# Kernel optimization log

Measured on AMD Instinct MI355X. Metric: run time of the kernel, lower is better.

## Reference

```python
import jax, jax.numpy as jnp
import numpy as np

N_NODES = 50000
N_EDGES = 800000
D = 64
E_DIM = 16
N_GRAPHS = 5000
BN_EPS = 1e-5


def _xavier(key, shape):
    fan_in, fan_out = shape[0], shape[1]
    limit = np.sqrt(6.0 / (fan_in + fan_out))
    return jax.random.uniform(key, shape, jnp.float32, -limit, limit)


def setup_inputs() -> dict:
    key = jax.random.key(0)
    ks = jax.random.split(key, 16)
    x = jax.random.normal(ks[0], (N_NODES, D), jnp.float32)
    edge_index = jax.random.randint(ks[1], (2, N_EDGES), 0, N_NODES, jnp.int64)
    edge_attr = jax.random.normal(ks[2], (N_EDGES, E_DIM), jnp.float32)
    batch = jnp.sort(jax.random.randint(ks[3], (N_NODES,), 0, N_GRAPHS, jnp.int64))
    zdim = 2 * D + E_DIM  # 144
    params = {
        'fw0': _xavier(ks[4], (zdim, D)), 'fb0': jnp.zeros((D,), jnp.float32),
        'sw0': _xavier(ks[5], (zdim, D)), 'sb0': jnp.zeros((D,), jnp.float32),
        'bng0': jnp.ones((D,), jnp.float32), 'bnb0': jnp.zeros((D,), jnp.float32),
        'fw1': _xavier(ks[6], (zdim, D)), 'fb1': jnp.zeros((D,), jnp.float32),
        'sw1': _xavier(ks[7], (zdim, D)), 'sb1': jnp.zeros((D,), jnp.float32),
        'bng1': jnp.ones((D,), jnp.float32), 'bnb1': jnp.zeros((D,), jnp.float32),
        'pw1': _xavier(ks[8], (D, D)), 'pb1': jnp.zeros((D,), jnp.float32),
        'pw2': _xavier(ks[9], (D, D)), 'pb2': jnp.zeros((D,), jnp.float32),
    }
    return dict(x=x, edge_index=edge_index, edge_attr=edge_attr, batch=batch, **params)


def _cgconv(x, src, dst, e, Wf, bf, Ws, bs):
    # PyG CGConv: x_i' = x_i + sum_j sigmoid(Wf z) * softplus(Ws z), z=[x_i, x_j, e]
    # edge_index[0]=source j, edge_index[1]=target i; aggregate at target.
    z = jnp.concatenate([x[dst], x[src], e], axis=-1)  # [E, 2D+Ed]
    m = jax.nn.sigmoid(z @ Wf + bf) * jax.nn.softplus(z @ Ws + bs)  # [E, D]
    agg = jax.ops.segment_sum(m, dst, num_segments=x.shape[0])
    return x + agg


def _batchnorm(x, gamma, beta):
    mu = jnp.mean(x, axis=0)
    var = jnp.mean(jnp.square(x - mu), axis=0)  # biased, training-mode BN
    return (x - mu) * jax.lax.rsqrt(var + BN_EPS) * gamma + beta


def reference(x, edge_index, edge_attr, batch,
              fw0, fb0, sw0, sb0, bng0, bnb0,
              fw1, fb1, sw1, sb1, bng1, bnb1,
              pw1, pb1, pw2, pb2):
    src, dst = edge_index[0], edge_index[1]
    h = _batchnorm(_cgconv(x, src, dst, edge_attr, fw0, fb0, sw0, sb0), bng0, bnb0)
    h = _batchnorm(_cgconv(h, src, dst, edge_attr, fw1, fb1, sw1, sb1), bng1, bnb1)
    # global mean pool over graphs
    sums = jax.ops.segment_sum(h, batch, num_segments=N_GRAPHS)
    cnt = jax.ops.segment_sum(jnp.ones((h.shape[0],), h.dtype), batch, num_segments=N_GRAPHS)
    pooled = sums / jnp.maximum(cnt, 1.0)[:, None]  # [G, D]
    # proj head: Linear -> LeakyReLU(0.01) -> Linear
    y = jax.nn.leaky_relu(pooled @ pw1 + pb1, negative_slope=0.01)
    return y @ pw2 + pb2
```

## Files before the change

### kernel.cpp

```cpp
#include <hip/hip_runtime.h>

#define NN 50000
#define NE 800000
#define DD 64
#define ED 16
#define NG 5000
#define SS 32

__global__ __launch_bounds__(256) void prep_weights(
    const float* __restrict__ fw0, const float* __restrict__ sw0,
    const float* __restrict__ fw1, const float* __restrict__ sw1,
    float2* __restrict__ Wd0, float2* __restrict__ Wsc0, float2* __restrict__ We0,
    float2* __restrict__ Wd1, float2* __restrict__ Wsc1, float2* __restrict__ We1) {
  int i = blockIdx.x * 256 + threadIdx.x;
  if (i >= 2 * 144 * 64) return;
  int layer = i >= 144 * 64;
  int j = i - layer * 144 * 64;
  int k = j >> 6, d = j & 63;
  const float* fw = layer ? fw1 : fw0;
  const float* sw = layer ? sw1 : sw0;
  float2 v = make_float2(fw[j], sw[j]);
  float2* Wd = layer ? Wd1 : Wd0;
  float2* Wsc = layer ? Wsc1 : Wsc0;
  float2* We = layer ? We1 : We0;
  if (k < 64)       Wd[k * DD + d] = v;
  else if (k < 128) Wsc[(k - 64) * DD + d] = v;
  else              We[(k - 128) * DD + d] = v;
}

__global__ __launch_bounds__(256) void k_hist(const int* __restrict__ ei,
                                              int* __restrict__ deg) {
  int e = blockIdx.x * 256 + threadIdx.x;
  if (e < NE) atomicAdd(&deg[ei[NE + e]], 1);
}

__global__ __launch_bounds__(256) void k_scan1(const int* __restrict__ deg,
                                               int* __restrict__ rowptr,
                                               int* __restrict__ partials) {
  __shared__ int sm[256];
  int t = threadIdx.x, i = blockIdx.x * 256 + t;
  int v = (i < NN) ? deg[i] : 0;
  sm[t] = v; __syncthreads();
  for (int off = 1; off < 256; off <<= 1) {
    int x = (t >= off) ? sm[t - off] : 0;
    __syncthreads();
    sm[t] += x;
    __syncthreads();
  }
  if (i < NN) rowptr[i] = sm[t] - v;
  if (t == 255) partials[blockIdx.x] = sm[255];
}

__global__ __launch_bounds__(256) void k_scan2(int* __restrict__ partials,
                                               int* __restrict__ poff, int nparts) {
  __shared__ int sm[256];
  int t = threadIdx.x;
  int v = (t < nparts) ? partials[t] : 0;
  sm[t] = v; __syncthreads();
  for (int off = 1; off < 256; off <<= 1) {
    int x = (t >= off) ? sm[t - off] : 0;
    __syncthreads();
    sm[t] += x;
    __syncthreads();
  }
  poff[t] = sm[t] - v;
}

__global__ __launch_bounds__(256) void k_scan3(int* __restrict__ rowptr,
                                               int* __restrict__ cursor,
                                               const int* __restrict__ poff) {
  int i = blockIdx.x * 256 + threadIdx.x;
  if (i < NN) {
    int v = rowptr[i] + poff[blockIdx.x];
    rowptr[i] = v;
    cursor[i] = v;
  } else if (i == NN) {
    rowptr[NN] = NE;
  }
}

__global__ __launch_bounds__(256) void k_scatter(const int* __restrict__ ei,
                                                 const float4* __restrict__ ea4,
                                                 int* __restrict__ cursor,
                                                 int* __restrict__ ssrc,
                                                 int* __restrict__ sdst,
                                                 float4* __restrict__ sea4) {
  int e = blockIdx.x * 256 + threadIdx.x;
  if (e >= NE) return;
  int dst = ei[NE + e];
  int pos = atomicAdd(&cursor[dst], 1);
  ssrc[pos] = ei[e];
  sdst[pos] = dst;
  const float4* q = ea4 + (size_t)e * 4;
  float4 a0 = q[0], a1 = q[1], a2 = q[2], a3 = q[3];
  float4* o = sea4 + (size_t)pos * 4;
  o[0] = a0; o[1] = a1; o[2] = a2; o[3] = a3;
}

template <int BN>
__global__ __launch_bounds__(256) void node_transform(
    const float* __restrict__ hin, const float* __restrict__ stats,
    const float* __restrict__ gamma, const float* __restrict__ beta,
    const float2* __restrict__ Wd, const float2* __restrict__ Wsc,
    const float* __restrict__ bf, const float* __restrict__ sbv,
    float2* __restrict__ Dst, float2* __restrict__ Src,
    float* __restrict__ hcopy) {
  __shared__ float hrow[32][DD];
  int tid = threadIdx.x, w = tid >> 6, d = tid & 63;
  int nbase = blockIdx.x * 32;
  const float invN = 1.f / (float)NN;
#pragma unroll
  for (int j = 0; j < 2; ++j) {
    int i4 = tid + j * 256;
    int node = nbase + (i4 >> 4);
    if (node < NN) {
      int c = (i4 & 15) * 4;
      float4 v = *(const float4*)(hin + (size_t)node * DD + c);
      if (BN) {
        float mu0 = stats[c + 0] * invN, va0 = stats[64 + c + 0] * invN - mu0 * mu0;
        float mu1 = stats[c + 1] * invN, va1 = stats[64 + c + 1] * invN - mu1 * mu1;
        float mu2 = stats[c + 2] * invN, va2 = stats[64 + c + 2] * invN - mu2 * mu2;
        float mu3 = stats[c + 3] * invN, va3 = stats[64 + c + 3] * invN - mu3 * mu3;
        float sc0 = rsqrtf(va0 + 1e-5f) * gamma[c + 0];
        float sc1 = rsqrtf(va1 + 1e-5f) * gamma[c + 1];
        float sc2 = rsqrtf(va2 + 1e-5f) * gamma[c + 2];
        float sc3 = rsqrtf(va3 + 1e-5f) * gamma[c + 3];
        v.x = fmaf(v.x, sc0, beta[c + 0] - mu0 * sc0);
        v.y = fmaf(v.y, sc1, beta[c + 1] - mu1 * sc1);
        v.z = fmaf(v.z, sc2, beta[c + 2] - mu2 * sc2);
        v.w = fmaf(v.w, sc3, beta[c + 3] - mu3 * sc3);
      }
      *(float4*)(&hrow[i4 >> 4][c]) = v;
      *(float4*)(hcopy + (size_t)node * DD + c) = v;
    }
  }
  __syncthreads();

  float bfd = bf[d], sbd = sbv[d];
  float2 ad[8], as_[8];
#pragma unroll
  for (int i = 0; i < 8; ++i) { ad[i] = make_float2(bfd, sbd); as_[i] = make_float2(0.f, 0.f); }

  for (int kk = 0; kk < 16; ++kk) {
    int k0 = kk * 4;
    float2 wd0 = Wd[(k0 + 0) * DD + d], wd1 = Wd[(k0 + 1) * DD + d];
    float2 wd2 = Wd[(k0 + 2) * DD + d], wd3 = Wd[(k0 + 3) * DD + d];
    float2 ws0 = Wsc[(k0 + 0) * DD + d], ws1 = Wsc[(k0 + 1) * DD + d];
    float2 ws2 = Wsc[(k0 + 2) * DD + d], ws3 = Wsc[(k0 + 3) * DD + d];
#pragma unroll
    for (int i = 0; i < 8; ++i) {
      float4 hv = *(const float4*)(&hrow[w * 8 + i][k0]);
      ad[i].x = fmaf(hv.x, wd0.x, ad[i].x); ad[i].y = fmaf(hv.x, wd0.y, ad[i].y);
      as_[i].x = fmaf(hv.x, ws0.x, as_[i].x); as_[i].y = fmaf(hv.x, ws0.y, as_[i].y);
      ad[i].x = fmaf(hv.y, wd1.x, ad[i].x); ad[i].y = fmaf(hv.y, wd1.y, ad[i].y);
      as_[i].x = fmaf(hv.y, ws1.x, as_[i].x); as_[i].y = fmaf(hv.y, ws1.y, as_[i].y);
      ad[i].x = fmaf(hv.z, wd2.x, ad[i].x); ad[i].y = fmaf(hv.z, wd2.y, ad[i].y);
      as_[i].x = fmaf(hv.z, ws2.x, as_[i].x); as_[i].y = fmaf(hv.z, ws2.y, as_[i].y);
      ad[i].x = fmaf(hv.w, wd3.x, ad[i].x); ad[i].y = fmaf(hv.w, wd3.y, ad[i].y);
      as_[i].x = fmaf(hv.w, ws3.x, as_[i].x); as_[i].y = fmaf(hv.w, ws3.y, as_[i].y);
    }
  }
#pragma unroll
  for (int i = 0; i < 8; ++i) {
    int n = nbase + w * 8 + i;
    if (n < NN) {
      Dst[(size_t)n * DD + d] = ad[i];
      Src[(size_t)n * DD + d] = as_[i];
    }
  }
}

__global__ __launch_bounds__(256, 6) void conv_strip(
    const int* __restrict__ ssrc, const int* __restrict__ sdst,
    const float4* __restrict__ sea4, const float2* __restrict__ We,
    const float2* __restrict__ Dst, const float2* __restrict__ Src,
    float* __restrict__ out) {
  __shared__ float4 sEA[4][SS * 4];
  __shared__ int sid[4][2 * SS];
  int tid = threadIdx.x, w = tid >> 6, d = tid & 63;
  int strip = blockIdx.x * 4 + w;
  int base = strip * SS;

  sEA[w][d]      = sea4[(size_t)base * 4 + d];
  sEA[w][64 + d] = sea4[(size_t)base * 4 + 64 + d];
  sid[w][d] = (d < SS) ? ssrc[base + d] : sdst[base + (d - SS)];
  __syncthreads();

  float2 we[16];
#pragma unroll
  for (int k = 0; k < 16; ++k) we[k] = We[k * DD + d];

  const char* SrcB = (const char*)Src;
  const char* DstB = (const char*)Dst;
  unsigned doff = (unsigned)d * 8u;

#define LOADSRC(n) (*(const float2*)(SrcB + (((unsigned)(n)) << 9) + doff))
#define LOADDST(n) (*(const float2*)(DstB + (((unsigned)(n)) << 9) + doff))

  float2 bufA[4], bufB[4];
#pragma unroll
  for (int j = 0; j < 4; ++j) bufA[j] = LOADSRC(sid[w][j]);

  int curdst = sid[w][SS];
  float2 a = LOADDST(curdst);
  float acc = 0.f;

#pragma unroll
  for (int g = 0; g < SS / 4; ++g) {
    float2* cur = (g & 1) ? bufB : bufA;
    float2* nxt = (g & 1) ? bufA : bufB;
    if (g < SS / 4 - 1) {
#pragma unroll
      for (int j = 0; j < 4; ++j) nxt[j] = LOADSRC(sid[w][g * 4 + 4 + j]);
    }
#pragma unroll
    for (int j = 0; j < 4; ++j) {
      int i = g * 4 + j;
      int dstn = sid[w][SS + i];
      if (dstn != curdst) {
        atomicAdd(&out[(unsigned)curdst * 64u + (unsigned)d], acc);
        acc = 0.f;
        curdst = dstn;
        a = LOADDST(curdst);
      }
      float2 b = cur[j];
      float cf = a.x + b.x, cs = a.y + b.y;
#pragma unroll
      for (int k = 0; k < 4; ++k) {
        float4 z = sEA[w][i * 4 + k];
        cf = fmaf(z.x, we[4 * k + 0].x, cf); cs = fmaf(z.x, we[4 * k + 0].y, cs);
        cf = fmaf(z.y, we[4 * k + 1].x, cf); cs = fmaf(z.y, we[4 * k + 1].y, cs);
        cf = fmaf(z.z, we[4 * k + 2].x, cf); cs = fmaf(z.z, we[4 * k + 2].y, cs);
        cf = fmaf(z.w, we[4 * k + 3].x, cf); cs = fmaf(z.w, we[4 * k + 3].y, cs);
      }
      float sig = __builtin_amdgcn_rcpf(1.f + __expf(-cf));
      float sp  = fmaxf(cs, 0.f) + __logf(1.f + __expf(-fabsf(cs)));
      acc = fmaf(sig, sp, acc);
    }
  }
  atomicAdd(&out[(unsigned)curdst * 64u + (unsigned)d], acc);
#undef LOADSRC
#undef LOADDST
}

__global__ __launch_bounds__(256) void bn_stats(const float* __restrict__ h,
                                                float* __restrict__ stats) {
  int tid = threadIdx.x;
  int c = (tid & 15) * 4;
  int r0 = blockIdx.x * 16 + (tid >> 4);
  float4 s = make_float4(0, 0, 0, 0), ss = make_float4(0, 0, 0, 0);
  for (int r = r0; r < NN; r += gridDim.x * 16) {
    float4 v = *(const float4*)(h + (size_t)r * DD + c);
    s.x += v.x; s.y += v.y; s.z += v.z; s.w += v.w;
    ss.x += v.x * v.x; ss.y += v.y * v.y; ss.z += v.z * v.z; ss.w += v.w * v.w;
  }
  __shared__ float4 sm[256], sm2[256];
  sm[tid] = s; sm2[tid] = ss;
  __syncthreads();
  for (int str = 128; str >= 16; str >>= 1) {
    if (tid < str) {
      sm[tid].x += sm[tid + str].x; sm[tid].y += sm[tid + str].y;
      sm[tid].z += sm[tid + str].z; sm[tid].w += sm[tid + str].w;
      sm2[tid].x += sm2[tid + str].x; sm2[tid].y += sm2[tid + str].y;
      sm2[tid].z += sm2[tid + str].z; sm2[tid].w += sm2[tid + str].w;
    }
    __syncthreads();
  }
  if (tid < 16) {
    int cc = tid * 4;
    atomicAdd(&stats[cc + 0], sm[tid].x); atomicAdd(&stats[cc + 1], sm[tid].y);
    atomicAdd(&stats[cc + 2], sm[tid].z); atomicAdd(&stats[cc + 3], sm[tid].w);
    atomicAdd(&stats[64 + cc + 0], sm2[tid].x); atomicAdd(&stats[64 + cc + 1], sm2[tid].y);
    atomicAdd(&stats[64 + cc + 2], sm2[tid].z); atomicAdd(&stats[64 + cc + 3], sm2[tid].w);
  }
}

__global__ __launch_bounds__(256) void pool_bn(
    const float* __restrict__ h, const int* __restrict__ batch,
    const float* __restrict__ stats,
    const float* __restrict__ gamma, const float* __restrict__ beta,
    float* __restrict__ psum, float* __restrict__ pcnt) {
  int tid = threadIdx.x, g = tid >> 6, d = tid & 63;
  const float invN = 1.f / (float)NN;
  float mu = stats[d] * invN;
  float var = stats[64 + d] * invN - mu * mu;
  float sc = rsqrtf(var + 1e-5f) * gamma[d];
  float sh = beta[d] - mu * sc;
  int n0 = (blockIdx.x * 4 + g) * 32;
  if (n0 >= NN) return;
  int nend = n0 + 32; if (nend > NN) nend = NN;
  int bprev = batch[n0];
  float acc = 0.f; int run = 0;
  for (int n = n0; n < nend; ++n) {
    int b = batch[n];
    if (b != bprev) {
      atomicAdd(&psum[(size_t)bprev * DD + d], acc);
      if (d == 0) atomicAdd(&pcnt[bprev], (float)run);
      acc = 0.f; run = 0; bprev = b;
    }
    acc += fmaf(h[(size_t)n * DD + d], sc, sh);
    ++run;
  }
  atomicAdd(&psum[(size_t)bprev * DD + d], acc);
  if (d == 0) atomicAdd(&pcnt[bprev], (float)run);
}

__global__ __launch_bounds__(256) void head_kernel(
    const float* __restrict__ psum, const float* __restrict__ pcnt,
    const float* __restrict__ pw1, const float* __restrict__ pb1,
    const float* __restrict__ pw2, const float* __restrict__ pb2,
    float* __restrict__ out) {
  __shared__ float row[4][DD], y1[4][DD];
  int tid = threadIdx.x, g = tid >> 6, d = tid & 63;
  int q = blockIdx.x * 4 + g;
  float c = fmaxf(pcnt[q], 1.0f);
  row[g][d] = psum[(size_t)q * DD + d] * __builtin_amdgcn_rcpf(c);
  __syncthreads();
  float acc = pb1[d];
#pragma unroll
  for (int k = 0; k < DD; ++k) acc = fmaf(row[g][k], pw1[k * DD + d], acc);
  acc = acc > 0.f ? acc : 0.01f * acc;
  y1[g][d] = acc;
  __syncthreads();
  float o = pb2[d];
#pragma unroll
  for (int k = 0; k < DD; ++k) o = fmaf(y1[g][k], pw2[k * DD + d], o);
  out[(size_t)q * DD + d] = o;
}

extern "C" void kernel_launch(void* const* d_in, const int* in_sizes, int n_in,
                              void* d_out, int out_size, void* d_ws, size_t ws_size,
                              hipStream_t stream) {
  const float* x     = (const float*)d_in[0];
  const int*   ei    = (const int*)d_in[1];
  const float* ea    = (const float*)d_in[2];
  const int*   batch = (const int*)d_in[3];
  const float* fw0 = (const float*)d_in[4],  *fb0 = (const float*)d_in[5];
  const float* sw0 = (const float*)d_in[6],  *sb0 = (const float*)d_in[7];
  const float* bng0= (const float*)d_in[8],  *bnb0= (const float*)d_in[9];
  const float* fw1 = (const float*)d_in[10], *fb1 = (const float*)d_in[11];
  const float* sw1 = (const float*)d_in[12], *sb1 = (const float*)d_in[13];
  const float* bng1= (const float*)d_in[14], *bnb1= (const float*)d_in[15];
  const float* pw1 = (const float*)d_in[16], *pb1 = (const float*)d_in[17];
  const float* pw2 = (const float*)d_in[18], *pb2 = (const float*)d_in[19];

  const size_t NND = (size_t)NN * DD;
  float4* sea4 = (float4*)d_ws;
  float2* Wd0  = (float2*)(sea4 + (size_t)NE * 4);
  float2* Wsc0 = Wd0 + 64 * DD;
  float2* We0  = Wsc0 + 64 * DD;
  float2* Wd1  = We0 + ED * DD;
  float2* Wsc1 = Wd1 + 64 * DD;
  float2* We1  = Wsc1 + 64 * DD;
  float2* Dst  = We1 + ED * DD;
  float2* Src  = Dst + NND;
  float*  h1   = (float*)(Src + NND);
  float*  h2   = h1 + NND;
  int*    deg    = (int*)(h2 + NND);
  float*  stats0 = (float*)(deg + NN);
  float*  stats1 = stats0 + 256;
  float*  psum   = stats1 + 256;
  float*  pcnt   = psum + (size_t)NG * DD;
  int* rowptr   = (int*)(pcnt + NG);
  int* cursor   = rowptr + NN + 1;
  int* partials = cursor + NN;
  int* poff     = partials + 256;
  int* ssrc     = poff + 256;
  int* sdst     = ssrc + NE;

  const int NB_NODE = (NN + 255) / 256;

  hipMemsetAsync(deg, 0,
                 ((size_t)NN + 512 + (size_t)NG * DD + NG) * sizeof(float), stream);
  prep_weights<<<72, 256, 0, stream>>>(fw0, sw0, fw1, sw1,
                                       Wd0, Wsc0, We0, Wd1, Wsc1, We1);

  k_hist<<<(NE + 255) / 256, 256, 0, stream>>>(ei, deg);
  k_scan1<<<NB_NODE, 256, 0, stream>>>(deg, rowptr, partials);
  k_scan2<<<1, 256, 0, stream>>>(partials, poff, NB_NODE);
  k_scan3<<<(NN + 256) / 256, 256, 0, stream>>>(rowptr, cursor, poff);
  k_scatter<<<(NE + 255) / 256, 256, 0, stream>>>(ei, (const float4*)ea, cursor,
                                                  ssrc, sdst, sea4);

  node_transform<0><<<(NN + 31) / 32, 256, 0, stream>>>(
      x, nullptr, nullptr, nullptr, Wd0, Wsc0, fb0, sb0, Dst, Src, h1);
  conv_strip<<<NE / SS / 4, 256, 0, stream>>>(ssrc, sdst, sea4, We0, Dst, Src, h1);
  bn_stats<<<128, 256, 0, stream>>>(h1, stats0);

  node_transform<1><<<(NN + 31) / 32, 256, 0, stream>>>(
      h1, stats0, bng0, bnb0, Wd1, Wsc1, fb1, sb1, Dst, Src, h2);
  conv_strip<<<NE / SS / 4, 256, 0, stream>>>(ssrc, sdst, sea4, We1, Dst, Src, h2);
  bn_stats<<<128, 256, 0, stream>>>(h2, stats1);

  pool_bn<<<391, 256, 0, stream>>>(h2, batch, stats1, bng1, bnb1, psum, pcnt);
  head_kernel<<<NG / 4, 256, 0, stream>>>(psum, pcnt, pw1, pb1, pw2, pb2, (float*)d_out);
}
```

Before: 578.5 us.

## Replace edge scatter with rank-based inverse permutation and indirect edge gathers

The histogram kernel now records each edge's atomic rank. A new kernel builds an inverse permutation from rowptr plus rank, so the physical copy of sorted src/dst/edge_attr arrays is gone. Each conv_strip pass instead gathers edge ids, endpoints and edge attributes through the permutation. This drops the 51 MB sorted edge_attr write and its reads, but turns the conv reads into random 64-byte gathers done twice, once per layer.

```diff
diff --git a/kernel.cpp b/kernel.cpp
--- a/kernel.cpp
+++ b/kernel.cpp
@@ -28,10 +28,11 @@
   else              We[(k - 128) * DD + d] = v;
 }
 
-__global__ __launch_bounds__(256) void k_hist(const int* __restrict__ ei,
-                                              int* __restrict__ deg) {
+__global__ __launch_bounds__(256) void k_hist_rank(const int* __restrict__ ei,
+                                                   int* __restrict__ deg,
+                                                   int* __restrict__ rank) {
   int e = blockIdx.x * 256 + threadIdx.x;
-  if (e < NE) atomicAdd(&deg[ei[NE + e]], 1);
+  if (e < NE) rank[e] = atomicAdd(&deg[ei[NE + e]], 1);
 }
 
 __global__ __launch_bounds__(256) void k_scan1(const int* __restrict__ deg,
@@ -67,34 +68,20 @@
 }
 
 __global__ __launch_bounds__(256) void k_scan3(int* __restrict__ rowptr,
-                                               int* __restrict__ cursor,
                                                const int* __restrict__ poff) {
   int i = blockIdx.x * 256 + threadIdx.x;
-  if (i < NN) {
-    int v = rowptr[i] + poff[blockIdx.x];
-    rowptr[i] = v;
-    cursor[i] = v;
-  } else if (i == NN) {
-    rowptr[NN] = NE;
-  }
-}
-
-__global__ __launch_bounds__(256) void k_scatter(const int* __restrict__ ei,
-                                                 const float4* __restrict__ ea4,
-                                                 int* __restrict__ cursor,
-                                                 int* __restrict__ ssrc,
-                                                 int* __restrict__ sdst,
-                                                 float4* __restrict__ sea4) {
+  if (i < NN) rowptr[i] += poff[blockIdx.x];
+  else if (i == NN) rowptr[NN] = NE;
+}
+
+__global__ __launch_bounds__(256) void k_inv(const int* __restrict__ ei,
+                                             const int* __restrict__ rowptr,
+                                             const int* __restrict__ rank,
+                                             int* __restrict__ inv) {
   int e = blockIdx.x * 256 + threadIdx.x;
   if (e >= NE) return;
-  int dst = ei[NE + e];
-  int pos = atomicAdd(&cursor[dst], 1);
-  ssrc[pos] = ei[e];
-  sdst[pos] = dst;
-  const float4* q = ea4 + (size_t)e * 4;
-  float4 a0 = q[0], a1 = q[1], a2 = q[2], a3 = q[3];
-  float4* o = sea4 + (size_t)pos * 4;
-  o[0] = a0; o[1] = a1; o[2] = a2; o[3] = a3;
+  int pos = rowptr[ei[NE + e]] + rank[e];
+  inv[pos] = e;
 }
 
 template <int BN>
@@ -171,20 +158,31 @@
 }
 
 __global__ __launch_bounds__(256, 6) void conv_strip(
-    const int* __restrict__ ssrc, const int* __restrict__ sdst,
-    const float4* __restrict__ sea4, const float2* __restrict__ We,
+    const int* __restrict__ inv, const int* __restrict__ ei,
+    const float4* __restrict__ ea4, const float2* __restrict__ We,
     const float2* __restrict__ Dst, const float2* __restrict__ Src,
     float* __restrict__ out) {
   __shared__ float4 sEA[4][SS * 4];
   __shared__ int sid[4][2 * SS];
+  __shared__ int se[4][SS];
   int tid = threadIdx.x, w = tid >> 6, d = tid & 63;
   int strip = blockIdx.x * 4 + w;
   int base = strip * SS;
 
-  sEA[w][d]      = sea4[(size_t)base * 4 + d];
-  sEA[w][64 + d] = sea4[(size_t)base * 4 + 64 + d];
-  sid[w][d] = (d < SS) ? ssrc[base + d] : sdst[base + (d - SS)];
-  __syncthreads();
+  if (d < SS) {
+    int e = inv[base + d];
+    se[w][d] = e;
+    sid[w][d] = ei[e];
+    sid[w][SS + d] = ei[NE + e];
+  }
+  __syncthreads();
+
+#pragma unroll
+  for (int r = 0; r < 2; ++r) {
+    int idx = r * 64 + d;
+    int e = se[w][idx >> 2];
+    sEA[w][idx] = ea4[(size_t)e * 4 + (idx & 3)];
+  }
 
   float2 we[16];
 #pragma unroll
@@ -204,6 +202,7 @@
   int curdst = sid[w][SS];
   float2 a = LOADDST(curdst);
   float acc = 0.f;
+  __syncthreads();
 
 #pragma unroll
   for (int g = 0; g < SS / 4; ++g) {
@@ -345,8 +344,7 @@
   const float* pw2 = (const float*)d_in[18], *pb2 = (const float*)d_in[19];
 
   const size_t NND = (size_t)NN * DD;
-  float4* sea4 = (float4*)d_ws;
-  float2* Wd0  = (float2*)(sea4 + (size_t)NE * 4);
+  float2* Wd0  = (float2*)d_ws;
   float2* Wsc0 = Wd0 + 64 * DD;
   float2* We0  = Wsc0 + 64 * DD;
   float2* Wd1  = We0 + ED * DD;
@@ -362,11 +360,10 @@
   float*  psum   = stats1 + 256;
   float*  pcnt   = psum + (size_t)NG * DD;
   int* rowptr   = (int*)(pcnt + NG);
-  int* cursor   = rowptr + NN + 1;
-  int* partials = cursor + NN;
+  int* partials = rowptr + NN + 1;
   int* poff     = partials + 256;
-  int* ssrc     = poff + 256;
-  int* sdst     = ssrc + NE;
+  int* rank     = poff + 256;
+  int* inv      = rank + NE;
 
   const int NB_NODE = (NN + 255) / 256;
 
@@ -375,21 +372,22 @@
   prep_weights<<<72, 256, 0, stream>>>(fw0, sw0, fw1, sw1,
                                        Wd0, Wsc0, We0, Wd1, Wsc1, We1);
 
-  k_hist<<<(NE + 255) / 256, 256, 0, stream>>>(ei, deg);
+  k_hist_rank<<<(NE + 255) / 256, 256, 0, stream>>>(ei, deg, rank);
   k_scan1<<<NB_NODE, 256, 0, stream>>>(deg, rowptr, partials);
   k_scan2<<<1, 256, 0, stream>>>(partials, poff, NB_NODE);
-  k_scan3<<<(NN + 256) / 256, 256, 0, stream>>>(rowptr, cursor, poff);
-  k_scatter<<<(NE + 255) / 256, 256, 0, stream>>>(ei, (const float4*)ea, cursor,
-                                                  ssrc, sdst, sea4);
+  k_scan3<<<(NN + 256) / 256, 256, 0, stream>>>(rowptr, poff);
+  k_inv<<<(NE + 255) / 256, 256, 0, stream>>>(ei, rowptr, rank, inv);
 
   node_transform<0><<<(NN + 31) / 32, 256, 0, stream>>>(
       x, nullptr, nullptr, nullptr, Wd0, Wsc0, fb0, sb0, Dst, Src, h1);
-  conv_strip<<<NE / SS / 4, 256, 0, stream>>>(ssrc, sdst, sea4, We0, Dst, Src, h1);
+  conv_strip<<<NE / SS / 4, 256, 0, stream>>>(inv, ei, (const float4*)ea,
+                                              We0, Dst, Src, h1);
   bn_stats<<<128, 256, 0, stream>>>(h1, stats0);
 
   node_transform<1><<<(NN + 31) / 32, 256, 0, stream>>>(
       h1, stats0, bng0, bnb0, Wd1, Wsc1, fb1, sb1, Dst, Src, h2);
-  conv_strip<<<NE / SS / 4, 256, 0, stream>>>(ssrc, sdst, sea4, We1, Dst, Src, h2);
+  conv_strip<<<NE / SS / 4, 256, 0, stream>>>(inv, ei, (const float4*)ea,
+                                              We1, Dst, Src, h2);
   bn_stats<<<128, 256, 0, stream>>>(h2, stats1);
 
   pool_bn<<<391, 256, 0, stream>>>(h2, batch, stats1, bng1, bnb1, psum, pcnt);
```

Result: faster. 541.0 us (-6.5%).
